# Optimization experiments

Measured on AMD Instinct MI355X. Metric: run time of the kernel, lower is better.

Reference implementation:

```python
import jax, jax.numpy as jnp
import numpy as np
from jax import lax

H = 2048      # hidden_size
S = 8192      # seq_len (single packed sequence, batch=1)
HK = 8        # num_key_heads
HV = 16       # num_value_heads
DK = 128      # key_head_dim
DV = 128      # value_head_dim
KCONV = 4     # conv kernel size
CHUNK = 64    # chunk size for gated delta rule
EPS = 1e-6    # rms_norm_eps / l2norm eps
CONV_DIM = 2 * HK * DK + HV * DV  # 4096


def setup_inputs() -> dict:
    key = jax.random.key(0)
    ks = jax.random.split(key, 9)
    def w(k, shape, scale):
        return jax.random.normal(k, shape, jnp.float32) * scale
    return {
        "hidden_states": jax.random.normal(ks[0], (1, S, H), jnp.float32),
        "W_qkv": w(ks[1], (H, CONV_DIM), H ** -0.5),
        "W_z": w(ks[2], (H, HV * DV), H ** -0.5),
        "W_b": w(ks[3], (H, HV), H ** -0.5),
        "W_a": w(ks[4], (H, HV), H ** -0.5),
        "conv_w": w(ks[5], (CONV_DIM, KCONV), KCONV ** -0.5),  # depthwise, weight.squeeze(1)
        "A_log": jnp.log(jax.random.uniform(ks[6], (HV,), jnp.float32, 1e-2, 16.0)),
        "dt_bias": jnp.ones((HV,), jnp.float32),
        "norm_w": jnp.ones((DV,), jnp.float32),
        "W_out": w(ks[7], (HV * DV, H), (HV * DV) ** -0.5),
    }


def _l2norm(x):
    return x * lax.rsqrt(jnp.sum(x * x, axis=-1, keepdims=True) + EPS)


def _chunk_gated_delta_rule(q, k, v, g, beta):
    # q,k: [S,Hv,DK]; v: [S,Hv,DV]; g,beta: [S,Hv]. use_qk_l2norm_in_kernel=True.
    scale = DK ** -0.5
    q = _l2norm(q) * scale
    k = _l2norm(k)
    v = v * beta[..., None]
    k_beta = k * beta[..., None]
    n = S // CHUNK
    def chunkify(x):
        return x.reshape(n, CHUNK, HV, x.shape[-1]).transpose(0, 2, 1, 3)  # [n,Hv,C,d]
    q, k, v, k_beta = map(chunkify, (q, k, v, k_beta))
    g = jnp.cumsum(g.reshape(n, CHUNK, HV).transpose(0, 2, 1), axis=-1)  # [n,Hv,C]
    tril_s = jnp.tril(jnp.ones((CHUNK, CHUNK), bool), -1)   # strictly lower
    tril = jnp.tril(jnp.ones((CHUNK, CHUNK), bool))         # incl diagonal
    diff = g[..., :, None] - g[..., None, :]                 # [n,Hv,C,C]
    neg_inf = jnp.float32(-1e30)
    # WY representation: T = (I - A)^{-1}, A strictly lower
    A = -jnp.einsum('nhid,nhjd->nhij', k_beta, k) * jnp.exp(jnp.where(tril_s, diff, neg_inf))
    A = jnp.where(tril_s, A, 0.0)
    T = jnp.linalg.inv(jnp.eye(CHUNK, dtype=A.dtype) - A)    # [n,Hv,C,C]
    w_ = jnp.einsum('nhij,nhjv->nhiv', T, v)                 # "value" in ref
    u_ = jnp.einsum('nhij,nhjk->nhik', T, k_beta * jnp.exp(g)[..., None])  # k_cumdecay
    Aqk = jnp.einsum('nhid,nhjd->nhij', q, k) * jnp.exp(jnp.where(tril, diff, neg_inf))
    g_exp = jnp.exp(g)
    g_last = g[..., -1]

    def step(state, inp):  # state: [Hv,DK,DV]
        q_i, k_i, Aqk_i, w_i, u_i, gexp_i, glast_i, g_i = inp
        v_prime = jnp.einsum('hck,hkv->hcv', u_i, state)
        v_new = w_i - v_prime
        o_inter = jnp.einsum('hck,hkv->hcv', q_i * gexp_i[..., None], state)
        o_i = o_inter + jnp.einsum('hij,hjv->hiv', Aqk_i, v_new)
        k_dec = k_i * jnp.exp(glast_i[:, None] - g_i)[..., None]
        state = state * jnp.exp(glast_i)[:, None, None] + jnp.einsum('hck,hcv->hkv', k_dec, v_new)
        return state, o_i

    state0 = jnp.zeros((HV, DK, DV), q.dtype)
    _, o = lax.scan(step, state0, (q, k, Aqk, w_, u_, g_exp, g_last, g))  # o: [n,Hv,C,DV]
    return o.transpose(0, 2, 1, 3).reshape(S, HV, DV)


def reference(hidden_states, W_qkv, W_z, W_b, W_a, conv_w, A_log, dt_bias, norm_w, W_out):
    x = hidden_states[0]                       # [S,H], batch==1
    mixed = x @ W_qkv                          # [S,CONV_DIM]
    z = (x @ W_z).reshape(S, HV, DV)
    b = x @ W_b                                # [S,HV]
    a = x @ W_a                                # [S,HV]
    # causal depthwise conv1d (padding=K-1, truncate) + silu
    xp = jnp.pad(mixed, ((KCONV - 1, 0), (0, 0)))
    conv = sum(xp[j:j + S] * conv_w[None, :, j] for j in range(KCONV))
    mixed = jax.nn.silu(conv)
    q, k, v = jnp.split(mixed, [HK * DK, 2 * HK * DK], axis=-1)
    q = q.reshape(S, HK, DK)
    k = k.reshape(S, HK, DK)
    v = v.reshape(S, HV, DV)
    beta = jax.nn.sigmoid(b)                   # [S,HV]
    g = -jnp.exp(A_log) * jax.nn.softplus(a + dt_bias)  # [S,HV]
    rep = HV // HK
    q = jnp.repeat(q, rep, axis=1)             # [S,HV,DK]
    k = jnp.repeat(k, rep, axis=1)
    core = _chunk_gated_delta_rule(q, k, v, g, beta)     # [S,HV,DV]
    # gated RMSNorm: rmsnorm(core) * w * silu(z)
    core = core * lax.rsqrt(jnp.mean(core * core, axis=-1, keepdims=True) + EPS)
    core = core * norm_w * jax.nn.silu(z)
    out = core.reshape(S, HV * DV) @ W_out     # [S,H]
    return out[None]                           # [1,S,H]
```

## Files before the change

### kernel.cpp

```cpp
#include <hip/hip_runtime.h>

#define S_LEN 8192
#define HID 2048
#define HKN 8
#define HVN 16
#define DKD 128
#define DVD 128
#define NCHUNK 128
#define CLEN 64
#define NQKV 4096
#define EPSF 1e-6f

typedef unsigned int u32;
typedef unsigned short u16;
typedef __attribute__((ext_vector_type(8))) short s16x8;
typedef __attribute__((ext_vector_type(4))) float f32x4;

__device__ __forceinline__ float bfraw2f(u16 v) { return __uint_as_float(((u32)v) << 16); }
__device__ __forceinline__ u16 f2bf_rne(float f) {
    u32 u = __float_as_uint(f);
    u32 r = u + 0x7fffu + ((u >> 16) & 1u);
    return (u16)(r >> 16);
}
__device__ __forceinline__ void unpack8(uint4 u, float* f) {
    const u32 a[4] = {u.x, u.y, u.z, u.w};
#pragma unroll
    for (int q = 0; q < 4; ++q) {
        f[2*q]   = __uint_as_float(a[q] << 16);
        f[2*q+1] = __uint_as_float(a[q] & 0xffff0000u);
    }
}
__device__ __forceinline__ uint4 pack8(const float* v) {
    uint4 r;
    r.x = (u32)f2bf_rne(v[0]) | ((u32)f2bf_rne(v[1]) << 16);
    r.y = (u32)f2bf_rne(v[2]) | ((u32)f2bf_rne(v[3]) << 16);
    r.z = (u32)f2bf_rne(v[4]) | ((u32)f2bf_rne(v[5]) << 16);
    r.w = (u32)f2bf_rne(v[6]) | ((u32)f2bf_rne(v[7]) << 16);
    return r;
}

__device__ __forceinline__ void gload_lds16(const u16* g, u16* l) {
    __builtin_amdgcn_global_load_lds((const __attribute__((address_space(1))) unsigned int*)g,
                                     (__attribute__((address_space(3))) unsigned int*)l, 16, 0, 0);
}
__device__ __forceinline__ void gload_lds4(const float* g, u16* l) {
    __builtin_amdgcn_global_load_lds((const __attribute__((address_space(1))) unsigned int*)g,
                                     (__attribute__((address_space(3))) unsigned int*)l, 4, 0, 0);
}

__global__ __launch_bounds__(256) void ba_kernel(const float* __restrict__ x,
                                                 const float* __restrict__ Wb,
                                                 const float* __restrict__ Wa,
                                                 const float* __restrict__ A_log,
                                                 const float* __restrict__ dt_bias,
                                                 float* __restrict__ beta,
                                                 float* __restrict__ g) {
    const int t = threadIdx.x;
    const int row = blockIdx.x * 8 + (t >> 5);
    const int c = t & 31;
    const int cc = c & 15;
    const float* W = (c < 16) ? Wb : Wa;
    const float* xr = x + (size_t)row * HID;
    float acc = 0.f;
    for (int k = 0; k < HID; ++k) acc = fmaf(xr[k], W[k * 16 + cc], acc);
    if (c < 16) {
        beta[row * 16 + cc] = 1.f / (1.f + expf(-acc));
    } else {
        float v = acc + dt_bias[cc];
        float sp = (v > 20.f) ? v : log1pf(expf(v));
        g[row * 16 + cc] = -expf(A_log[cc]) * sp;
    }
}

__global__ __launch_bounds__(256) void cvt_x_kernel(const float* __restrict__ x,
                                                    u16* __restrict__ xb) {
    const size_t i8 = ((size_t)blockIdx.x * 256 + threadIdx.x) << 3;
    float4 a = *(const float4*)(x + i8);
    float4 b = *(const float4*)(x + i8 + 4);
    float v[8] = {a.x, a.y, a.z, a.w, b.x, b.y, b.z, b.w};
    *(uint4*)(xb + i8) = pack8(v);
}

__global__ __launch_bounds__(256) void cvt_wT_kernel(const float* __restrict__ W,
                                                     u16* __restrict__ Wt,
                                                     int N, int K) {
    __shared__ u16 T[64 * 72];
    const int t = threadIdx.x;
    const int n0 = blockIdx.x * 64;
    const int k0 = blockIdx.y * 64;
#pragma unroll
    for (int i = 0; i < 4; ++i) {
        int flat = i * 256 + t;
        int kr = flat >> 4, c4 = (flat & 15) << 2;
        float4 v = *(const float4*)(W + (size_t)(k0 + kr) * N + n0 + c4);
        T[(c4 + 0) * 72 + kr] = f2bf_rne(v.x);
        T[(c4 + 1) * 72 + kr] = f2bf_rne(v.y);
        T[(c4 + 2) * 72 + kr] = f2bf_rne(v.z);
        T[(c4 + 3) * 72 + kr] = f2bf_rne(v.w);
    }
    __syncthreads();
#pragma unroll
    for (int i = 0; i < 2; ++i) {
        int flat = i * 256 + t;
        int n = flat >> 3, k8 = (flat & 7) << 3;
        *(uint4*)(Wt + (size_t)(n0 + n) * K + k0 + k8) = *(const uint4*)(T + n * 72 + k8);
    }
}

template <int F32OUT>
__global__ __launch_bounds__(256) void gemm_bt(const u16* __restrict__ A,
                                               const u16* __restrict__ Bt,
                                               void* __restrict__ Cv,
                                               int M, int N, int K) {
    __shared__ __align__(16) u16 As[128 * 64];
    __shared__ __align__(16) u16 Bs[128 * 64];
    const int t = threadIdx.x;
    const int n0 = blockIdx.x * 128;
    const int m0 = blockIdx.y * 128;
    const int w = t >> 6, lane = t & 63;
    const int wm = (w >> 1) * 64, wn = (w & 1) * 64;
    const int ml = lane & 15, kq = lane >> 4;
    f32x4 acc[4][4];
#pragma unroll
    for (int i = 0; i < 4; ++i)
#pragma unroll
        for (int j = 0; j < 4; ++j) acc[i][j] = (f32x4){0.f, 0.f, 0.f, 0.f};

    for (int k0 = 0; k0 < K; k0 += 64) {
#pragma unroll
        for (int r = 0; r < 4; ++r) {
            int flat = r * 256 + t;
            int row = flat >> 3, kc = (flat & 7) << 3;
            gload_lds16(A  + (size_t)(m0 + row) * K + k0 + kc, As + flat * 8);
            gload_lds16(Bt + (size_t)(n0 + row) * K + k0 + kc, Bs + flat * 8);
        }
        __syncthreads();
#pragma unroll
        for (int ks = 0; ks < 2; ++ks) {
            s16x8 af[4], bfr[4];
#pragma unroll
            for (int mt = 0; mt < 4; ++mt)
                af[mt] = *(const s16x8*)(As + (wm + mt * 16 + ml) * 64 + ks * 32 + kq * 8);
#pragma unroll
            for (int nt = 0; nt < 4; ++nt)
                bfr[nt] = *(const s16x8*)(Bs + (wn + nt * 16 + ml) * 64 + ks * 32 + kq * 8);
#pragma unroll
            for (int mt = 0; mt < 4; ++mt)
#pragma unroll
                for (int nt = 0; nt < 4; ++nt)
                    acc[mt][nt] = __builtin_amdgcn_mfma_f32_16x16x32_bf16(af[mt], bfr[nt], acc[mt][nt], 0, 0, 0);
        }
        __syncthreads();
    }
#pragma unroll
    for (int mt = 0; mt < 4; ++mt)
#pragma unroll
        for (int nt = 0; nt < 4; ++nt)
#pragma unroll
            for (int r = 0; r < 4; ++r) {
                int row = m0 + wm + mt * 16 + kq * 4 + r;
                int col = n0 + wn + nt * 16 + ml;
                float v = acc[mt][nt][r];
                if (F32OUT)
                    ((float*)Cv)[(size_t)row * N + col] = v;
                else
                    ((u16*)Cv)[(size_t)row * N + col] = f2bf_rne(v);
            }
}

__global__ __launch_bounds__(512) void prep_kernel(const u16* __restrict__ Cmix,
                                                   const float* __restrict__ conv_w,
                                                   const float* __restrict__ beta,
                                                   u16* __restrict__ qn,
                                                   u16* __restrict__ kn,
                                                   u16* __restrict__ vb) {
    const int s = blockIdx.x;
    const int t = threadIdx.x;
    const int c8 = t << 3;
    __shared__ float ssq[16];
    if (t < 16) ssq[t] = 0.f;

    float y[8];
#pragma unroll
    for (int i = 0; i < 8; ++i) y[i] = 0.f;
    {
        uint4 mrow[4];
#pragma unroll
        for (int j = 0; j < 4; ++j) {
            int r = s - 3 + j;
            if (r >= 0) mrow[j] = *(const uint4*)(Cmix + (size_t)r * NQKV + c8);
            else        mrow[j] = uint4{0u, 0u, 0u, 0u};
        }
        float cw[8][4];
#pragma unroll
        for (int i = 0; i < 8; ++i) {
            float4 cv = *(const float4*)(conv_w + (size_t)(c8 + i) * 4);
            cw[i][0] = cv.x; cw[i][1] = cv.y; cw[i][2] = cv.z; cw[i][3] = cv.w;
        }
#pragma unroll
        for (int j = 0; j < 4; ++j) {
            float mf[8];
            unpack8(mrow[j], mf);
#pragma unroll
            for (int i = 0; i < 8; ++i) y[i] = fmaf(mf[i], cw[i][j], y[i]);
        }
#pragma unroll
        for (int i = 0; i < 8; ++i) {
            float v = y[i];
            y[i] = v / (1.f + expf(-v));
        }
    }
    __syncthreads();
    if (t < 256) {
        float p = 0.f;
#pragma unroll
        for (int i = 0; i < 8; ++i) p += y[i] * y[i];
        atomicAdd(&ssq[t >> 4], p);
    }
    __syncthreads();
    if (t < 128) {
        float rn = rsqrtf(ssq[t >> 4] + EPSF) * 0.08838834764831845f;
        float ov[8];
#pragma unroll
        for (int i = 0; i < 8; ++i) ov[i] = y[i] * rn;
        *(uint4*)(qn + (size_t)s * 1024 + c8) = pack8(ov);
    } else if (t < 256) {
        float rn = rsqrtf(ssq[t >> 4] + EPSF);
        float ov[8];
#pragma unroll
        for (int i = 0; i < 8; ++i) ov[i] = y[i] * rn;
        *(uint4*)(kn + (size_t)s * 1024 + (c8 - 1024)) = pack8(ov);
    } else {
        int vh = (c8 - 2048) >> 7;
        float bb = beta[s * 16 + vh];
        float ov[8];
#pragma unroll
        for (int i = 0; i < 8; ++i) ov[i] = y[i] * bb;
        *(uint4*)(vb + (size_t)s * 2048 + (c8 - 2048)) = pack8(ov);
    }
}

__global__ __launch_bounds__(256, 2) void precomp_kernel(const u16* __restrict__ qn,
                                                         const u16* __restrict__ kn,
                                                         const u16* __restrict__ vb,
                                                         const float* __restrict__ g,
                                                         const float* __restrict__ beta,
                                                         u16* __restrict__ bufB,
                                                         u16* __restrict__ bufK,
                                                         float* __restrict__ egc_arr,
                                                         float* __restrict__ ekd_arr,
                                                         float* __restrict__ eg) {
    const int b = blockIdx.x;
    const int n = b >> 4, h = b & 15, hs = h >> 1;
    const int t = threadIdx.x;
    const int s0 = n * 64;
    u16* BB = bufB + (size_t)b * 20480;

    __shared__ __align__(16) u16 sK[64 * 128];
    __shared__ __align__(16) u16 sVQ[64 * 128];
    __shared__ __align__(16) u16 sKT[64 * 128];
    __shared__ __align__(16) float Am[64 * 64];
    __shared__ float gc[64], bet[64], bexp[64];

    const int w = t >> 6, l = t & 63;
    const int l15 = l & 15, l4 = l >> 4;

#pragma unroll
    for (int i = 0; i < 4; ++i) {
        int flat = i * 256 + t;
        int c = flat >> 4, dc = (flat & 15) << 3;
        int sw = c * 128 + ((((dc >> 3) ^ (c & 7))) << 3);
        *(uint4*)(sK + sw)  = *(const uint4*)(kn + (size_t)(s0 + c) * 1024 + hs * 128 + dc);
        *(uint4*)(sVQ + sw) = *(const uint4*)(vb + (size_t)(s0 + c) * 2048 + h * 128 + dc);
    }
    if (t < 64) {
        gc[t] = g[(size_t)(s0 + t) * 16 + h];
        bet[t] = beta[(size_t)(s0 + t) * 16 + h];
    }
    __syncthreads();
    if (t == 0) {
        float run = 0.f;
        for (int c = 0; c < 64; ++c) { run += gc[c]; gc[c] = run; }
    }
    __syncthreads();
    if (t < 64) {
        float e = expf(gc[t]);
        float ek = expf(gc[63] - gc[t]);
        bexp[t] = bet[t] * e;
        egc_arr[b * 64 + t] = e;
        ekd_arr[b * 64 + t] = ek;
    }
    if (t == 0) eg[b] = expf(gc[63]);
    __syncthreads();

    {
        s16x8 ak[4];
#pragma unroll
        for (int kk = 0; kk < 4; ++kk)
            ak[kk] = *(const s16x8*)(sK + (w * 16 + l15) * 128 + (((kk * 4 + l4) ^ (l15 & 7)) << 3));
        for (int nt = 0; nt <= w; ++nt) {
            f32x4 acc = (f32x4){0.f, 0.f, 0.f, 0.f};
#pragma unroll
            for (int kk = 0; kk < 4; ++kk) {
                s16x8 bk = *(const s16x8*)(sK + (nt * 16 + l15) * 128 + (((kk * 4 + l4) ^ (l15 & 7)) << 3));
                acc = __builtin_amdgcn_mfma_f32_16x16x32_bf16(ak[kk], bk, acc, 0, 0, 0);
            }
            const int j = nt * 16 + l15;
#pragma unroll
            for (int r = 0; r < 4; ++r) {
                int i = w * 16 + l4 * 4 + r;
                if (j < i) Am[i * 64 + j] = -acc[r] * bet[i] * expf(gc[i] - gc[j]);
            }
        }
    }
    uint4 vreg[4];
    {
        const int c = t & 63, db = t >> 6;
#pragma unroll
        for (int r = 0; r < 4; ++r) {
            uint4 kv = *(const uint4*)(sK + c * 128 + ((((4 * db + r) ^ (c & 7))) << 3));
            const u16* kp = (const u16*)&kv;
#pragma unroll
            for (int e = 0; e < 8; ++e) {
                int d = (4 * db + r) * 8 + e;
                sKT[d * 64 + ((((c >> 3) ^ (d & 7))) << 3) + (c & 7)] = kp[e];
            }
            vreg[r] = *(const uint4*)(sVQ + c * 128 + ((((4 * db + r) ^ (c & 7))) << 3));
        }
    }
    __syncthreads();

    {
        const int c = t & 63, db = t >> 6;
#pragma unroll
        for (int r = 0; r < 4; ++r) {
            const u16* vp = (const u16*)&vreg[r];
#pragma unroll
            for (int e = 0; e < 8; ++e) {
                int d = (4 * db + r) * 8 + e;
                sVQ[d * 64 + ((((c >> 3) ^ (d & 7))) << 3) + (c & 7)] = vp[e];
            }
        }
    }
    __syncthreads();

    if (t < 64) {
        float Tc[64];
#pragma unroll
        for (int i = 0; i < 64; ++i) {
            float val = (t == i) ? 1.f : 0.f;
#pragma unroll
            for (int j = 0; j < i; ++j) val = fmaf(Am[i * 64 + j], Tc[j], val);
            Tc[i] = val;
            Am[i * 64 + t] = val;
        }
    }
    __syncthreads();

    float tv[16];
    {
        const int c = t >> 2, j0 = (t & 3) << 4;
#pragma unroll
        for (int q = 0; q < 16; ++q) tv[q] = Am[c * 64 + j0 + q];
    }
    {
        u16* KB = bufK + (size_t)((n << 3) + hs) * 16384;
#pragma unroll
        for (int i = 0; i < 4; ++i) {
            int f = t * 4 + i;
            int d = f >> 3, sb = f & 7;
            uint4 v = *(const uint4*)(sKT + d * 64 + sb * 8);
            if ((h & 1) == 0) *(uint4*)(KB + 8192 + d * 64 + sb * 8) = v;
            int jb = ((sb ^ (d & 7)) << 3);
            float vf[8]; unpack8(v, vf);
#pragma unroll
            for (int e = 0; e < 8; ++e) vf[e] *= bexp[jb + e];
            *(uint4*)(sKT + d * 64 + sb * 8) = pack8(vf);
        }
    }
    __syncthreads();

    {
        u16* Tb = (u16*)Am;
        const int c = t >> 2, j0 = (t & 3) << 4;
        uint4 p0 = pack8(tv), p1 = pack8(tv + 8);
        *(uint4*)(Tb + c * 64 + ((((j0 >> 3) ^ (c & 7))) << 3)) = p0;
        *(uint4*)(Tb + c * 64 + (((((j0 >> 3) + 1) ^ (c & 7))) << 3)) = p1;
    }
    __syncthreads();

    {
        const u16* Tb = (const u16*)Am;
#pragma unroll
        for (int fr2 = 0; fr2 < 2; ++fr2) {
            const int d = w * 32 + fr2 * 16 + l15;
            s16x8 au[2];
#pragma unroll
            for (int kk = 0; kk < 2; ++kk)
                au[kk] = *(const s16x8*)(sKT + d * 64 + (((kk * 4 + l4) ^ (d & 7)) << 3));
#pragma unroll
            for (int fc = 0; fc < 4; ++fc) {
                const int c = fc * 16 + l15;
                f32x4 acc = (f32x4){0.f, 0.f, 0.f, 0.f};
#pragma unroll
                for (int kk = 0; kk < 2; ++kk) {
                    s16x8 bt = *(const s16x8*)(Tb + c * 64 + (((kk * 4 + l4) ^ (c & 7)) << 3));
                    acc = __builtin_amdgcn_mfma_f32_16x16x32_bf16(au[kk], bt, acc, 0, 0, 0);
                }
                const int d0 = w * 32 + fr2 * 16 + l4 * 4;
                uint2 pr;
                pr.x = (u32)f2bf_rne(-acc[0]) | ((u32)f2bf_rne(-acc[1]) << 16);
                pr.y = (u32)f2bf_rne(-acc[2]) | ((u32)f2bf_rne(-acc[3]) << 16);
                *(uint2*)(BB + 8192 + c * 128 + (((d0 >> 3) ^ (c & 7)) << 3) + (d0 & 7)) = pr;
            }
        }
#pragma unroll
        for (int fc2 = 0; fc2 < 2; ++fc2) {
            const int dv = w * 32 + fc2 * 16 + l15;
            s16x8 bv[2];
#pragma unroll
            for (int kk = 0; kk < 2; ++kk)
                bv[kk] = *(const s16x8*)(sVQ + dv * 64 + (((kk * 4 + l4) ^ (dv & 7)) << 3));
#pragma unroll
            for (int fr = 0; fr < 4; ++fr) {
                const int c = fr * 16 + l15;
                f32x4 acc = (f32x4){0.f, 0.f, 0.f, 0.f};
#pragma unroll
                for (int kk = 0; kk < 2; ++kk) {
                    s16x8 at = *(const s16x8*)(Tb + c * 64 + (((kk * 4 + l4) ^ (c & 7)) << 3));
                    acc = __builtin_amdgcn_mfma_f32_16x16x32_bf16(at, bv[kk], acc, 0, 0, 0);
                }
                const int c0 = fr * 16 + l4 * 4;
                uint2 pr;
                pr.x = (u32)f2bf_rne(acc[0]) | ((u32)f2bf_rne(acc[1]) << 16);
                pr.y = (u32)f2bf_rne(acc[2]) | ((u32)f2bf_rne(acc[3]) << 16);
                *(uint2*)(BB + dv * 64 + c0) = pr;
            }
        }
    }
    __syncthreads();

#pragma unroll
    for (int i = 0; i < 4; ++i) {
        int flat = i * 256 + t;
        int c = flat >> 4, dc = (flat & 15) << 3;
        *(uint4*)(sKT + c * 128 + ((((dc >> 3) ^ (c & 7))) << 3)) =
            *(const uint4*)(qn + (size_t)(s0 + c) * 1024 + hs * 128 + dc);
    }
    __syncthreads();

    {
        const u16* sQ = sKT;
        s16x8 aq[4];
#pragma unroll
        for (int kk = 0; kk < 4; ++kk)
            aq[kk] = *(const s16x8*)(sQ + (w * 16 + l15) * 128 + (((kk * 4 + l4) ^ (l15 & 7)) << 3));
#pragma unroll
        for (int nt = 0; nt < 4; ++nt) {
            f32x4 acc = (f32x4){0.f, 0.f, 0.f, 0.f};
            if (nt <= w) {
#pragma unroll
                for (int kk = 0; kk < 4; ++kk) {
                    s16x8 bk = *(const s16x8*)(sK + (nt * 16 + l15) * 128 + (((kk * 4 + l4) ^ (l15 & 7)) << 3));
                    acc = __builtin_amdgcn_mfma_f32_16x16x32_bf16(aq[kk], bk, acc, 0, 0, 0);
                }
            }
            const int jj = nt * 16 + l15;
#pragma unroll
            for (int r = 0; r < 4; ++r) {
                const int i = w * 16 + l4 * 4 + r;
                float val = 0.f;
                if (nt < w || (nt == w && jj <= i)) val = acc[r] * expf(gc[i] - gc[jj]);
                BB[16384 + i * 64 + (((jj >> 3) ^ (i & 7)) << 3) + (jj & 7)] = f2bf_rne(val);
            }
        }
        if ((h & 1) == 0) {
            u16* KB = bufK + (size_t)((n << 3) + hs) * 16384;
#pragma unroll
            for (int i = 0; i < 4; ++i) {
                int f = i * 256 + t;
                int c = f >> 4, sb = f & 15;
                *(uint4*)(KB + c * 128 + sb * 8) = *(const uint4*)(sQ + c * 128 + sb * 8);
            }
        }
    }
}

#define STG 28928
#define OFF_AQK 8192
#define OFF_QA 12288
#define OFF_KA 20480
#define OFF_EGC 28672
#define OFF_EKD 28800

__global__ __launch_bounds__(256, 1) void scan_kernel(const u16* __restrict__ bufB,
                                                      const u16* __restrict__ bufK,
                                                      const float* __restrict__ egc_g,
                                                      const float* __restrict__ ekd_g,
                                                      const float* __restrict__ eg_g,
                                                      u16* __restrict__ o) {
    __shared__ __align__(16) u16 sStage[2 * STG];
    __shared__ __align__(16) u16 sSTb[4][16 * 136];
    __shared__ __align__(16) u16 sVT[4][16 * 72];
    __shared__ __align__(16) u16 sVTs[4][16 * 72];

    const int h = blockIdx.x >> 1;
    const int dvh = (blockIdx.x & 1) << 6;
    const int hs = h >> 1;
    const int w = threadIdx.x >> 6;
    const int l = threadIdx.x & 63;
    const int l15 = l & 15, l4 = l >> 4, l7 = l & 7;
    const int dv0 = dvh + (w << 4);

    u16* STb = sSTb[w];
    u16* VT  = sVT[w];
    u16* VTs = sVTs[w];

    for (int i = l; i < 16 * 136; i += 64) STb[i] = 0;

    f32x4 Sreg[8];
#pragma unroll
    for (int i = 0; i < 8; ++i) Sreg[i] = (f32x4){0.f, 0.f, 0.f, 0.f};

    auto stage = [&](int n2, u16* dst) {
        const int b2 = (n2 << 4) + h;
        const u16* sA = bufB + (size_t)b2 * 20480 + 8192 + (w * 3072 + l * 8);
        u16* dA = dst + w * 3072;
#pragma unroll
        for (int i = 0; i < 6; ++i) gload_lds16(sA + i * 512, dA + i * 512);
        const u16* sB = bufK + (size_t)((n2 << 3) + hs) * 16384 + (w * 4096 + l * 8);
        u16* dB = dst + 12288 + w * 4096;
#pragma unroll
        for (int i = 0; i < 8; ++i) gload_lds16(sB + i * 512, dB + i * 512);
        if (w == 0) gload_lds4(egc_g + (b2 << 6) + l, dst + OFF_EGC);
        else if (w == 1) gload_lds4(ekd_g + (b2 << 6) + l, dst + OFF_EKD);
    };
    auto loadW = [&](int n2, uint2 (&wr)[4]) {
        const u16* wb = bufB + (size_t)((n2 << 4) + h) * 20480 + (size_t)(dv0 + l15) * 64 + l4 * 4;
#pragma unroll
        for (int mt = 0; mt < 4; ++mt) wr[mt] = *(const uint2*)(wb + mt * 16);
    };

    uint2 wA[4], wB[4];
    float egA, egB;
    stage(0, sStage);
    loadW(0, wA);
    egA = eg_g[h];
    __syncthreads();

    int cur = 0;
    for (int n = 0; n < NCHUNK; ++n) {
        const u16* buf = sStage + cur * STG;
        if (n + 1 < NCHUNK) {
            stage(n + 1, sStage + (cur ^ 1) * STG);
            loadW(n + 1, wB);
            egB = eg_g[((n + 1) << 4) + h];
        }
        const u16* bU = buf;
        const u16* bA = buf + OFF_AQK;
        const u16* bQ = buf + OFF_QA;
        const u16* bK = buf + OFF_KA;
        const float* egc = (const float*)(buf + OFF_EGC);
        const float* ekd = (const float*)(buf + OFF_EKD);

        s16x8 bF[4];
#pragma unroll
        for (int kk = 0; kk < 4; ++kk)
            bF[kk] = *(const s16x8*)(STb + l15 * 136 + kk * 32 + l4 * 8);

        f32x4 V[4];
#pragma unroll
        for (int mt = 0; mt < 4; ++mt) {
            V[mt][0] = bfraw2f((u16)(wA[mt].x & 0xffffu));
            V[mt][1] = bfraw2f((u16)(wA[mt].x >> 16));
            V[mt][2] = bfraw2f((u16)(wA[mt].y & 0xffffu));
            V[mt][3] = bfraw2f((u16)(wA[mt].y >> 16));
        }
#pragma unroll
        for (int kk = 0; kk < 4; ++kk) {
            const int sw = ((kk * 4 + l4) ^ l7) << 3;
#pragma unroll
            for (int mt = 0; mt < 4; ++mt) {
                s16x8 a = *(const s16x8*)(bU + (mt * 16 + l15) * 128 + sw);
                V[mt] = __builtin_amdgcn_mfma_f32_16x16x32_bf16(a, bF[kk], V[mt], 0, 0, 0);
            }
        }

        f32x4 O[4];
#pragma unroll
        for (int mt = 0; mt < 4; ++mt) O[mt] = (f32x4){0.f, 0.f, 0.f, 0.f};
#pragma unroll
        for (int kk = 0; kk < 4; ++kk) {
            const int sw = ((kk * 4 + l4) ^ l7) << 3;
#pragma unroll
            for (int mt = 0; mt < 4; ++mt) {
                s16x8 a = *(const s16x8*)(bQ + (mt * 16 + l15) * 128 + sw);
                O[mt] = __builtin_amdgcn_mfma_f32_16x16x32_bf16(a, bF[kk], O[mt], 0, 0, 0);
            }
        }
#pragma unroll
        for (int mt = 0; mt < 4; ++mt)
#pragma unroll
            for (int r = 0; r < 4; ++r) O[mt][r] *= egc[mt * 16 + l4 * 4 + r];

#pragma unroll
        for (int mt = 0; mt < 4; ++mt) {
            const int cb = mt * 16 + l4 * 4;
            uint2 uv, us;
            uv.x = (u32)f2bf_rne(V[mt][0]) | ((u32)f2bf_rne(V[mt][1]) << 16);
            uv.y = (u32)f2bf_rne(V[mt][2]) | ((u32)f2bf_rne(V[mt][3]) << 16);
            us.x = (u32)f2bf_rne(V[mt][0] * ekd[cb]) | ((u32)f2bf_rne(V[mt][1] * ekd[cb + 1]) << 16);
            us.y = (u32)f2bf_rne(V[mt][2] * ekd[cb + 2]) | ((u32)f2bf_rne(V[mt][3] * ekd[cb + 3]) << 16);
            *(uint2*)(VT + l15 * 72 + cb) = uv;
            *(uint2*)(VTs + l15 * 72 + cb) = us;
        }

        s16x8 vF0 = *(const s16x8*)(VT + l15 * 72 + l4 * 8);
        s16x8 vF1 = *(const s16x8*)(VT + l15 * 72 + 32 + l4 * 8);
#pragma unroll
        for (int mt = 0; mt < 4; ++mt) {
            s16x8 a = *(const s16x8*)(bA + (mt * 16 + l15) * 64 + ((l4 ^ l7) << 3));
            O[mt] = __builtin_amdgcn_mfma_f32_16x16x32_bf16(a, vF0, O[mt], 0, 0, 0);
        }
#pragma unroll
        for (int mt = 0; mt < 4; ++mt) {
            s16x8 a = *(const s16x8*)(bA + (mt * 16 + l15) * 64 + (((4 + l4) ^ l7) << 3));
            O[mt] = __builtin_amdgcn_mfma_f32_16x16x32_bf16(a, vF1, O[mt], 0, 0, 0);
        }

        const int s0 = n << 6;
#pragma unroll
        for (int mt = 0; mt < 4; ++mt)
#pragma unroll
            for (int r = 0; r < 4; ++r)
                o[(size_t)(s0 + mt * 16 + l4 * 4 + r) * 2048 + (h << 7) + dv0 + l15] = f2bf_rne(O[mt][r]);

        s16x8 sF0 = *(const s16x8*)(VTs + l15 * 72 + l4 * 8);
        s16x8 sF1 = *(const s16x8*)(VTs + l15 * 72 + 32 + l4 * 8);
#pragma unroll
        for (int nt = 0; nt < 8; ++nt) {
#pragma unroll
            for (int r = 0; r < 4; ++r) Sreg[nt][r] *= egA;
            s16x8 a0 = *(const s16x8*)(bK + (nt * 16 + l15) * 64 + ((l4 ^ l7) << 3));
            Sreg[nt] = __builtin_amdgcn_mfma_f32_16x16x32_bf16(a0, sF0, Sreg[nt], 0, 0, 0);
            s16x8 a1 = *(const s16x8*)(bK + (nt * 16 + l15) * 64 + (((4 + l4) ^ l7) << 3));
            Sreg[nt] = __builtin_amdgcn_mfma_f32_16x16x32_bf16(a1, sF1, Sreg[nt], 0, 0, 0);
        }
#pragma unroll
        for (int nt = 0; nt < 8; ++nt) {
            uint2 sv;
            sv.x = (u32)f2bf_rne(Sreg[nt][0]) | ((u32)f2bf_rne(Sreg[nt][1]) << 16);
            sv.y = (u32)f2bf_rne(Sreg[nt][2]) | ((u32)f2bf_rne(Sreg[nt][3]) << 16);
            *(uint2*)(STb + l15 * 136 + nt * 16 + l4 * 4) = sv;
        }
        __syncthreads();
#pragma unroll
        for (int i = 0; i < 4; ++i) wA[i] = wB[i];
        egA = egB;
        cur ^= 1;
    }
}

__global__ __launch_bounds__(256) void gate_kernel(const u16* __restrict__ o,
                                                   const u16* __restrict__ Cz,
                                                   const float* __restrict__ norm_w,
                                                   u16* __restrict__ gated) {
    const int s = blockIdx.x, t = threadIdx.x;
    const int c8 = t << 3, hh = t >> 4;
    __shared__ float ssq[16];
    if (t < 16) ssq[t] = 0.f;
    float ov[8];
    unpack8(*(const uint4*)(o + (size_t)s * 2048 + c8), ov);
    float p = 0.f;
#pragma unroll
    for (int i = 0; i < 8; ++i) p += ov[i] * ov[i];
    __syncthreads();
    atomicAdd(&ssq[hh], p);
    __syncthreads();
    const float rms = rsqrtf(ssq[hh] * 0.0078125f + EPSF);
    float zf[8];
    unpack8(*(const uint4*)(Cz + (size_t)s * 2048 + c8), zf);
    const int d0 = c8 & 127;
    float res[8];
#pragma unroll
    for (int i = 0; i < 8; ++i) {
        float z = zf[i];
        float sz = z / (1.f + expf(-z));
        res[i] = ov[i] * rms * norm_w[d0 + i] * sz;
    }
    *(uint4*)(gated + (size_t)s * 2048 + c8) = pack8(res);
}

extern "C" void kernel_launch(void* const* d_in, const int* in_sizes, int n_in,
                              void* d_out, int out_size, void* d_ws, size_t ws_size,
                              hipStream_t stream) {
    (void)in_sizes; (void)n_in; (void)out_size; (void)ws_size;
    const float* x       = (const float*)d_in[0];
    const float* W_qkv   = (const float*)d_in[1];
    const float* W_z     = (const float*)d_in[2];
    const float* W_b     = (const float*)d_in[3];
    const float* W_a     = (const float*)d_in[4];
    const float* conv_w  = (const float*)d_in[5];
    const float* A_log   = (const float*)d_in[6];
    const float* dt_bias = (const float*)d_in[7];
    const float* norm_w  = (const float*)d_in[8];
    const float* W_out   = (const float*)d_in[9];

    char* p = (char*)d_ws;
    auto alloc = [&](size_t bytes) {
        char* r = p;
        p += (bytes + 255) & ~(size_t)255;
        return r;
    };
    u16* Cmix    = (u16*)alloc((size_t)S_LEN * NQKV * 2);
    char* extra  = alloc((size_t)50331648); (void)extra;
    u16* qn      = (u16*)alloc((size_t)S_LEN * HKN * DKD * 2);
    u16* kn      = (u16*)alloc((size_t)S_LEN * HKN * DKD * 2);
    u16* vb      = (u16*)alloc((size_t)S_LEN * HVN * DVD * 2);
    float* egc   = (float*)alloc((size_t)NCHUNK * HVN * CLEN * 4);
    float* ekd   = (float*)alloc((size_t)NCHUNK * HVN * CLEN * 4);
    float* eg    = (float*)alloc((size_t)NCHUNK * HVN * 4);
    float* beta  = (float*)alloc((size_t)S_LEN * HVN * 4);
    float* g     = (float*)alloc((size_t)S_LEN * HVN * 4);
    u16* bufB  = Cmix;
    u16* bufK  = (u16*)((char*)Cmix + (size_t)83886080);
    u16* o_buf = qn;
    u16* Cz    = vb;
    u16* gated = Cmix;
    u16* xbf    = (u16*)d_out;
    u16* Wq_t   = (u16*)d_out + (size_t)16777216;
    u16* Wz_t   = (u16*)d_out + (size_t)25165824;
    u16* Wout_t = qn;

    ba_kernel<<<S_LEN / 8, 256, 0, stream>>>(x, W_b, W_a, A_log, dt_bias, beta, g);
    cvt_x_kernel<<<S_LEN * HID / (256 * 8), 256, 0, stream>>>(x, xbf);
    cvt_wT_kernel<<<dim3(NQKV / 64, HID / 64), 256, 0, stream>>>(W_qkv, Wq_t, NQKV, HID);
    cvt_wT_kernel<<<dim3(HID / 64, HID / 64), 256, 0, stream>>>(W_z, Wz_t, HID, HID);
    gemm_bt<0><<<dim3(NQKV / 128, S_LEN / 128), 256, 0, stream>>>(xbf, Wq_t, Cmix, S_LEN, NQKV, HID);
    prep_kernel<<<S_LEN, 512, 0, stream>>>(Cmix, conv_w, beta, qn, kn, vb);
    precomp_kernel<<<NCHUNK * HVN, 256, 0, stream>>>(qn, kn, vb, g, beta, bufB, bufK, egc, ekd, eg);
    gemm_bt<0><<<dim3(HID / 128, S_LEN / 128), 256, 0, stream>>>(xbf, Wz_t, Cz, S_LEN, HID, HID);
    scan_kernel<<<HVN * 2, 256, 0, stream>>>(bufB, bufK, egc, ekd, eg, o_buf);
    gate_kernel<<<S_LEN, 256, 0, stream>>>(o_buf, Cz, norm_w, gated);
    cvt_wT_kernel<<<dim3(HID / 64, HID / 64), 256, 0, stream>>>(W_out, Wout_t, HID, HID);
    gemm_bt<1><<<dim3(HID / 128, S_LEN / 128), 256, 0, stream>>>(gated, Wout_t, d_out, S_LEN, HID, HID);
}
```

Baseline: 1.300 ms.

## Split sequential scan into state-only recurrence and parallel per-chunk output kernel

The scan kernel, which runs on only 32 workgroups, now carries just the recurrent state update and writes the bf16 state at the start of each chunk to a scratch buffer. A new kernel launched with one workgroup per (chunk, head) reads that stored state and computes the intra-chunk and inter-chunk outputs in parallel. This takes the output MFMAs and the global stores off the serial critical path. The cost is extra global traffic for the stored states and reloading the U/Q/A tiles. Separately, the GEMM remaps workgroup IDs in groups of eight, which changes which tiles run concurrently and is meant to improve cache locality.

```diff
diff --git a/kernel.cpp b/kernel.cpp
--- a/kernel.cpp
+++ b/kernel.cpp
@@ -115,8 +115,11 @@
     __shared__ __align__(16) u16 As[128 * 64];
     __shared__ __align__(16) u16 Bs[128 * 64];
     const int t = threadIdx.x;
-    const int n0 = blockIdx.x * 128;
-    const int m0 = blockIdx.y * 128;
+    const int nwg = gridDim.x * gridDim.y;
+    int bid = blockIdx.y * gridDim.x + blockIdx.x;
+    bid = (bid & 7) * (nwg >> 3) + (bid >> 3);
+    const int n0 = (bid % gridDim.x) * 128;
+    const int m0 = (bid / gridDim.x) * 128;
     const int w = t >> 6, lane = t & 63;
     const int wm = (w >> 1) * 64, wn = (w & 1) * 64;
     const int ml = lane & 15, kq = lane >> 4;
@@ -486,22 +489,15 @@
     }
 }
 
-#define STG 28928
-#define OFF_AQK 8192
-#define OFF_QA 12288
-#define OFF_KA 20480
-#define OFF_EGC 28672
-#define OFF_EKD 28800
-
-__global__ __launch_bounds__(256, 1) void scan_kernel(const u16* __restrict__ bufB,
-                                                      const u16* __restrict__ bufK,
-                                                      const float* __restrict__ egc_g,
-                                                      const float* __restrict__ ekd_g,
-                                                      const float* __restrict__ eg_g,
-                                                      u16* __restrict__ o) {
-    __shared__ __align__(16) u16 sStage[2 * STG];
+#define STGA 16512
+
+__global__ __launch_bounds__(256, 1) void scan_state_kernel(const u16* __restrict__ bufB,
+                                                            const u16* __restrict__ bufK,
+                                                            const float* __restrict__ ekd_g,
+                                                            const float* __restrict__ eg_g,
+                                                            u16* __restrict__ sstore) {
+    __shared__ __align__(16) u16 sStage[2 * STGA];
     __shared__ __align__(16) u16 sSTb[4][16 * 136];
-    __shared__ __align__(16) u16 sVT[4][16 * 72];
     __shared__ __align__(16) u16 sVTs[4][16 * 72];
 
     const int h = blockIdx.x >> 1;
@@ -513,7 +509,6 @@
     const int dv0 = dvh + (w << 4);
 
     u16* STb = sSTb[w];
-    u16* VT  = sVT[w];
     u16* VTs = sVTs[w];
 
     for (int i = l; i < 16 * 136; i += 64) STb[i] = 0;
@@ -524,16 +519,15 @@
 
     auto stage = [&](int n2, u16* dst) {
         const int b2 = (n2 << 4) + h;
-        const u16* sA = bufB + (size_t)b2 * 20480 + 8192 + (w * 3072 + l * 8);
-        u16* dA = dst + w * 3072;
-#pragma unroll
-        for (int i = 0; i < 6; ++i) gload_lds16(sA + i * 512, dA + i * 512);
-        const u16* sB = bufK + (size_t)((n2 << 3) + hs) * 16384 + (w * 4096 + l * 8);
-        u16* dB = dst + 12288 + w * 4096;
-#pragma unroll
-        for (int i = 0; i < 8; ++i) gload_lds16(sB + i * 512, dB + i * 512);
-        if (w == 0) gload_lds4(egc_g + (b2 << 6) + l, dst + OFF_EGC);
-        else if (w == 1) gload_lds4(ekd_g + (b2 << 6) + l, dst + OFF_EKD);
+        const u16* sU = bufB + (size_t)b2 * 20480 + 8192 + w * 2048 + l * 8;
+        u16* dU = dst + w * 2048;
+#pragma unroll
+        for (int i = 0; i < 4; ++i) gload_lds16(sU + i * 512, dU + i * 512);
+        const u16* sKa = bufK + (size_t)((n2 << 3) + hs) * 16384 + 8192 + w * 2048 + l * 8;
+        u16* dK = dst + 8192 + w * 2048;
+#pragma unroll
+        for (int i = 0; i < 4; ++i) gload_lds16(sKa + i * 512, dK + i * 512);
+        if (w == 0) gload_lds4(ekd_g + (b2 << 6) + l, dst + 16384);
     };
     auto loadW = [&](int n2, uint2 (&wr)[4]) {
         const u16* wb = bufB + (size_t)((n2 << 4) + h) * 20480 + (size_t)(dv0 + l15) * 64 + l4 * 4;
@@ -550,18 +544,24 @@
 
     int cur = 0;
     for (int n = 0; n < NCHUNK; ++n) {
-        const u16* buf = sStage + cur * STG;
+        const u16* buf = sStage + cur * STGA;
         if (n + 1 < NCHUNK) {
-            stage(n + 1, sStage + (cur ^ 1) * STG);
+            stage(n + 1, sStage + (cur ^ 1) * STGA);
             loadW(n + 1, wB);
             egB = eg_g[((n + 1) << 4) + h];
         }
+        if (n > 0) {
+            u16* dstg = sstore + ((size_t)(n * 16 + h)) * 16384 + (size_t)dv0 * 128;
+#pragma unroll
+            for (int i = 0; i < 4; ++i) {
+                int idx = l * 4 + i;
+                int row = idx >> 4, col = (idx & 15) << 3;
+                *(uint4*)(dstg + row * 128 + col) = *(const uint4*)(STb + row * 136 + col);
+            }
+        }
         const u16* bU = buf;
-        const u16* bA = buf + OFF_AQK;
-        const u16* bQ = buf + OFF_QA;
-        const u16* bK = buf + OFF_KA;
-        const float* egc = (const float*)(buf + OFF_EGC);
-        const float* ekd = (const float*)(buf + OFF_EKD);
+        const u16* bK = buf + 8192;
+        const float* ekd = (const float*)(buf + 16384);
 
         s16x8 bF[4];
 #pragma unroll
@@ -586,54 +586,14 @@
             }
         }
 
-        f32x4 O[4];
-#pragma unroll
-        for (int mt = 0; mt < 4; ++mt) O[mt] = (f32x4){0.f, 0.f, 0.f, 0.f};
-#pragma unroll
-        for (int kk = 0; kk < 4; ++kk) {
-            const int sw = ((kk * 4 + l4) ^ l7) << 3;
-#pragma unroll
-            for (int mt = 0; mt < 4; ++mt) {
-                s16x8 a = *(const s16x8*)(bQ + (mt * 16 + l15) * 128 + sw);
-                O[mt] = __builtin_amdgcn_mfma_f32_16x16x32_bf16(a, bF[kk], O[mt], 0, 0, 0);
-            }
-        }
-#pragma unroll
-        for (int mt = 0; mt < 4; ++mt)
-#pragma unroll
-            for (int r = 0; r < 4; ++r) O[mt][r] *= egc[mt * 16 + l4 * 4 + r];
-
 #pragma unroll
         for (int mt = 0; mt < 4; ++mt) {
             const int cb = mt * 16 + l4 * 4;
-            uint2 uv, us;
-            uv.x = (u32)f2bf_rne(V[mt][0]) | ((u32)f2bf_rne(V[mt][1]) << 16);
-            uv.y = (u32)f2bf_rne(V[mt][2]) | ((u32)f2bf_rne(V[mt][3]) << 16);
+            uint2 us;
             us.x = (u32)f2bf_rne(V[mt][0] * ekd[cb]) | ((u32)f2bf_rne(V[mt][1] * ekd[cb + 1]) << 16);
             us.y = (u32)f2bf_rne(V[mt][2] * ekd[cb + 2]) | ((u32)f2bf_rne(V[mt][3] * ekd[cb + 3]) << 16);
-            *(uint2*)(VT + l15 * 72 + cb) = uv;
             *(uint2*)(VTs + l15 * 72 + cb) = us;
         }
-
-        s16x8 vF0 = *(const s16x8*)(VT + l15 * 72 + l4 * 8);
-        s16x8 vF1 = *(const s16x8*)(VT + l15 * 72 + 32 + l4 * 8);
-#pragma unroll
-        for (int mt = 0; mt < 4; ++mt) {
-            s16x8 a = *(const s16x8*)(bA + (mt * 16 + l15) * 64 + ((l4 ^ l7) << 3));
-            O[mt] = __builtin_amdgcn_mfma_f32_16x16x32_bf16(a, vF0, O[mt], 0, 0, 0);
-        }
-#pragma unroll
-        for (int mt = 0; mt < 4; ++mt) {
-            s16x8 a = *(const s16x8*)(bA + (mt * 16 + l15) * 64 + (((4 + l4) ^ l7) << 3));
-            O[mt] = __builtin_amdgcn_mfma_f32_16x16x32_bf16(a, vF1, O[mt], 0, 0, 0);
-        }
-
-        const int s0 = n << 6;
-#pragma unroll
-        for (int mt = 0; mt < 4; ++mt)
-#pragma unroll
-            for (int r = 0; r < 4; ++r)
-                o[(size_t)(s0 + mt * 16 + l4 * 4 + r) * 2048 + (h << 7) + dv0 + l15] = f2bf_rne(O[mt][r]);
 
         s16x8 sF0 = *(const s16x8*)(VTs + l15 * 72 + l4 * 8);
         s16x8 sF1 = *(const s16x8*)(VTs + l15 * 72 + 32 + l4 * 8);
@@ -659,6 +619,118 @@
         egA = egB;
         cur ^= 1;
     }
+}
+
+__global__ __launch_bounds__(512, 4) void scan_out_kernel(const u16* __restrict__ bufB,
+                                                          const u16* __restrict__ bufK,
+                                                          const u16* __restrict__ sstore,
+                                                          const float* __restrict__ egc_g,
+                                                          u16* __restrict__ o) {
+    __shared__ __align__(16) u16 sStage[20608];
+    __shared__ __align__(16) u16 sVT[8][16 * 72];
+
+    const int bb = blockIdx.x;
+    const int n = bb >> 4, h = bb & 15, hs = h >> 1;
+    const int t = threadIdx.x;
+    const int w = t >> 6, l = t & 63;
+    const int l15 = l & 15, l4 = l >> 4, l7 = l & 7;
+    const int dv0 = w << 4;
+    u16* VT = sVT[w];
+
+#pragma unroll
+    for (int i = 0; i < 5; ++i) {
+        int c = w + i * 8;
+        if (c < 24)
+            gload_lds16(bufB + (size_t)bb * 20480 + 8192 + c * 512 + l * 8, sStage + c * 512);
+        else
+            gload_lds16(bufK + (size_t)((n << 3) + hs) * 16384 + (c - 24) * 512 + l * 8,
+                        sStage + 12288 + (c - 24) * 512);
+    }
+    if (w == 0) gload_lds4(egc_g + (bb << 6) + l, sStage + 20480);
+
+    uint2 wr[4];
+    {
+        const u16* wb = bufB + (size_t)bb * 20480 + (size_t)(dv0 + l15) * 64 + l4 * 4;
+#pragma unroll
+        for (int mt = 0; mt < 4; ++mt) wr[mt] = *(const uint2*)(wb + mt * 16);
+    }
+    s16x8 bF[4];
+    if (n > 0) {
+        const u16* sp = sstore + (size_t)bb * 16384 + (size_t)(dv0 + l15) * 128 + l4 * 8;
+#pragma unroll
+        for (int kk = 0; kk < 4; ++kk)
+            bF[kk] = *(const s16x8*)(sp + kk * 32);
+    }
+    __syncthreads();
+
+    const u16* bU = sStage;
+    const u16* bA = sStage + 8192;
+    const u16* qA = sStage + 12288;
+    const float* egc = (const float*)(sStage + 20480);
+
+    f32x4 V[4];
+#pragma unroll
+    for (int mt = 0; mt < 4; ++mt) {
+        V[mt][0] = bfraw2f((u16)(wr[mt].x & 0xffffu));
+        V[mt][1] = bfraw2f((u16)(wr[mt].x >> 16));
+        V[mt][2] = bfraw2f((u16)(wr[mt].y & 0xffffu));
+        V[mt][3] = bfraw2f((u16)(wr[mt].y >> 16));
+    }
+    f32x4 O[4];
+#pragma unroll
+    for (int mt = 0; mt < 4; ++mt) O[mt] = (f32x4){0.f, 0.f, 0.f, 0.f};
+    if (n > 0) {
+#pragma unroll
+        for (int kk = 0; kk < 4; ++kk) {
+            const int sw = ((kk * 4 + l4) ^ l7) << 3;
+#pragma unroll
+            for (int mt = 0; mt < 4; ++mt) {
+                s16x8 a = *(const s16x8*)(bU + (mt * 16 + l15) * 128 + sw);
+                V[mt] = __builtin_amdgcn_mfma_f32_16x16x32_bf16(a, bF[kk], V[mt], 0, 0, 0);
+            }
+        }
+#pragma unroll
+        for (int kk = 0; kk < 4; ++kk) {
+            const int sw = ((kk * 4 + l4) ^ l7) << 3;
+#pragma unroll
+            for (int mt = 0; mt < 4; ++mt) {
+                s16x8 a = *(const s16x8*)(qA + (mt * 16 + l15) * 128 + sw);
+                O[mt] = __builtin_amdgcn_mfma_f32_16x16x32_bf16(a, bF[kk], O[mt], 0, 0, 0);
+            }
+        }
+#pragma unroll
+        for (int mt = 0; mt < 4; ++mt)
+#pragma unroll
+            for (int r = 0; r < 4; ++r) O[mt][r] *= egc[mt * 16 + l4 * 4 + r];
+    }
+
+#pragma unroll
+    for (int mt = 0; mt < 4; ++mt) {
+        const int cb = mt * 16 + l4 * 4;
+        uint2 uv;
+        uv.x = (u32)f2bf_rne(V[mt][0]) | ((u32)f2bf_rne(V[mt][1]) << 16);
+        uv.y = (u32)f2bf_rne(V[mt][2]) | ((u32)f2bf_rne(V[mt][3]) << 16);
+        *(uint2*)(VT + l15 * 72 + cb) = uv;
+    }
+    s16x8 vF0 = *(const s16x8*)(VT + l15 * 72 + l4 * 8);
+    s16x8 vF1 = *(const s16x8*)(VT + l15 * 72 + 32 + l4 * 8);
+#pragma unroll
+    for (int mt = 0; mt < 4; ++mt) {
+        s16x8 a = *(const s16x8*)(bA + (mt * 16 + l15) * 64 + ((l4 ^ l7) << 3));
+        O[mt] = __builtin_amdgcn_mfma_f32_16x16x32_bf16(a, vF0, O[mt], 0, 0, 0);
+    }
+#pragma unroll
+    for (int mt = 0; mt < 4; ++mt) {
+        s16x8 a = *(const s16x8*)(bA + (mt * 16 + l15) * 64 + (((4 + l4) ^ l7) << 3));
+        O[mt] = __builtin_amdgcn_mfma_f32_16x16x32_bf16(a, vF1, O[mt], 0, 0, 0);
+    }
+
+    const int s0 = n << 6;
+#pragma unroll
+    for (int mt = 0; mt < 4; ++mt)
+#pragma unroll
+        for (int r = 0; r < 4; ++r)
+            o[(size_t)(s0 + mt * 16 + l4 * 4 + r) * 2048 + (h << 7) + dv0 + l15] = f2bf_rne(O[mt][r]);
 }
 
 __global__ __launch_bounds__(256) void gate_kernel(const u16* __restrict__ o,
@@ -730,6 +802,7 @@
     u16* xbf    = (u16*)d_out;
     u16* Wq_t   = (u16*)d_out + (size_t)16777216;
     u16* Wz_t   = (u16*)d_out + (size_t)25165824;
+    u16* sstore = (u16*)d_out;
     u16* Wout_t = qn;
 
     ba_kernel<<<S_LEN / 8, 256, 0, stream>>>(x, W_b, W_a, A_log, dt_bias, beta, g);
@@ -740,7 +813,8 @@
     prep_kernel<<<S_LEN, 512, 0, stream>>>(Cmix, conv_w, beta, qn, kn, vb);
     precomp_kernel<<<NCHUNK * HVN, 256, 0, stream>>>(qn, kn, vb, g, beta, bufB, bufK, egc, ekd, eg);
     gemm_bt<0><<<dim3(HID / 128, S_LEN / 128), 256, 0, stream>>>(xbf, Wz_t, Cz, S_LEN, HID, HID);
-    scan_kernel<<<HVN * 2, 256, 0, stream>>>(bufB, bufK, egc, ekd, eg, o_buf);
+    scan_state_kernel<<<HVN * 2, 256, 0, stream>>>(bufB, bufK, ekd, eg, sstore);
+    scan_out_kernel<<<NCHUNK * HVN, 512, 0, stream>>>(bufB, bufK, sstore, egc, o_buf);
     gate_kernel<<<S_LEN, 256, 0, stream>>>(o_buf, Cz, norm_w, gated);
     cvt_wT_kernel<<<dim3(HID / 64, HID / 64), 256, 0, stream>>>(W_out, Wout_t, HID, HID);
     gemm_bt<1><<<dim3(HID / 128, S_LEN / 128), 256, 0, stream>>>(gated, Wout_t, d_out, S_LEN, HID, HID);
```

Measured after the change: 1.227 ms. 5.6% less time.
